# Optimization experiments

Measured on AMD Instinct MI355X. Metric: run time of the kernel, lower is better.

## Reference

```python
import jax, jax.numpy as jnp
import numpy as np

# Pangu-Weather EarthSpecificBlock, layer-1 config
WZ, WH, WW = 2, 6, 12          # window size (z, lat, lon)
Z, H, W = 8, 91, 180           # token grid after patch embedding
C = 192                        # token dim
HEADS = 6
B = 1
PAD_TOP, PAD_BOT = 2, 3        # lat 91 -> 96 (CustomPad3d, centered)
ZP, HP, WP = 8, 96, 180        # padded grid
NWB = (ZP // WZ) * (HP // WH)  # 64 bias windows (z*lat)
N = WZ * WH * WW               # 144 tokens per window


def earth_position_index():
    zi = np.arange(WZ); zj = -np.arange(WZ) * WZ
    hi = np.arange(WH); hj = -np.arange(WH) * WH
    w = np.arange(WW)
    c1 = np.stack(np.meshgrid(zi, hi, w, indexing='ij')).reshape(3, -1)
    c2 = np.stack(np.meshgrid(zj, hj, w, indexing='ij')).reshape(3, -1)
    coords = (c1[:, :, None] - c2[:, None, :]).transpose(1, 2, 0).astype(np.int64)
    coords[:, :, 2] += WW - 1
    coords[:, :, 1] *= 2 * WW - 1
    coords[:, :, 0] *= (2 * WW - 1) * WH * WH
    return coords.sum(-1)  # (N, N) int indices into bias table

POS_IDX = jnp.asarray(earth_position_index())


def layer_norm(x, w, b, eps=1e-5):
    mu = x.mean(-1, keepdims=True)
    var = ((x - mu) ** 2).mean(-1, keepdims=True)
    return (x - mu) * jax.lax.rsqrt(var + eps) * w + b


def setup_inputs() -> dict:
    key = jax.random.key(0)
    ks = jax.random.split(key, 8)
    f = lambda k, s: jax.random.normal(k, s, jnp.float32) * 0.02
    return {
        "x": jax.random.normal(ks[0], (B, Z * H * W, C), jnp.float32),
        "qkv_w": f(ks[1], (3 * C, C)),
        "qkv_b": jnp.zeros((3 * C,), jnp.float32),
        "proj_w": f(ks[2], (C, C)),
        "proj_b": jnp.zeros((C,), jnp.float32),
        "bias_table": f(ks[3], ((2 * WW - 1) * WH * WH * WZ * WZ, NWB, HEADS)),
        "norm1_w": jnp.ones((C,), jnp.float32),
        "norm1_b": jnp.zeros((C,), jnp.float32),
        "norm2_w": jnp.ones((C,), jnp.float32),
        "norm2_b": jnp.zeros((C,), jnp.float32),
        "mlp_w1": f(ks[4], (4 * C, C)),
        "mlp_b1": jnp.zeros((4 * C,), jnp.float32),
        "mlp_w2": f(ks[5], (C, 4 * C)),
        "mlp_b2": jnp.zeros((C,), jnp.float32),
        "roll": 0,
    }


def reference(x, qkv_w, qkv_b, proj_w, proj_b, bias_table,
              norm1_w, norm1_b, norm2_w, norm2_b,
              mlp_w1, mlp_b1, mlp_w2, mlp_b2, roll):
    shortcut = x  # (B, L, C)
    hd = C // HEADS
    scale = hd ** -0.5
    xs = x.reshape(B, Z, H, W, C)
    xs = jnp.pad(xs, ((0, 0), (0, 0), (PAD_TOP, PAD_BOT), (0, 0), (0, 0)))
    # window partition: (B, ZP, HP, WP, C) -> (nb, N, C), windows ordered (z, lat, lon)
    xw = xs.reshape(B, ZP // WZ, WZ, HP // WH, WH, WP // WW, WW, C)
    xw = xw.transpose(0, 1, 3, 5, 2, 4, 6, 7).reshape(-1, N, C)
    nb = xw.shape[0]  # B * 64 * 15 = 960
    qkv = (xw @ qkv_w.T + qkv_b).reshape(nb, N, 3, HEADS, hd).transpose(2, 0, 3, 1, 4)
    q, k, v = qkv[0] * scale, qkv[1], qkv[2]  # each (nb, HEADS, N, hd)
    att = jnp.einsum('bhnd,bhmd->bhnm', q, k)  # (nb, HEADS, N, N)
    # earth-specific bias gathered via position index
    bias = bias_table[POS_IDX]                 # (N, N, NWB, HEADS)
    bias = bias.transpose(2, 3, 0, 1)          # (NWB, HEADS, N, N)
    # nb = B * NWB * n_lon_windows, NWB is the leading window factor
    att = att.reshape(B, NWB, -1, HEADS, N, N) + bias[None, :, None]
    att = jax.nn.softmax(att, axis=-1).reshape(nb, HEADS, N, N)
    out = jnp.einsum('bhnm,bhmd->bnhd', att, v).reshape(nb, N, C)
    out = out @ proj_w.T + proj_b
    # window reverse + crop padding
    out = out.reshape(B, ZP // WZ, HP // WH, WP // WW, WZ, WH, WW, C)
    out = out.transpose(0, 1, 4, 2, 5, 3, 6, 7).reshape(B, ZP, HP, WP, C)
    out = out[:, :, PAD_TOP:HP - PAD_BOT, :, :].reshape(B, -1, C)
    # post-norm residual (Pangu): x = shortcut + norm1(attn); x = x + norm2(mlp(x))
    x1 = shortcut + layer_norm(out, norm1_w, norm1_b)
    h1 = jax.nn.gelu(x1 @ mlp_w1.T + mlp_b1, approximate=False)
    mlp_out = h1 @ mlp_w2.T + mlp_b2
    return x1 + layer_norm(mlp_out, norm2_w, norm2_b)
```

## Files before the change

kernel.cpp:

```cpp
#include <hip/hip_runtime.h>
#include <hip/hip_bf16.h>

typedef __hip_bfloat16 bf16;
#define DEVI __device__ __forceinline__

typedef __bf16 bf16x8 __attribute__((ext_vector_type(8)));
typedef __bf16 bf16x4 __attribute__((ext_vector_type(4)));
typedef float  f32x4  __attribute__((ext_vector_type(4)));

DEVI float bf2f(bf16 v) { return __bfloat162float(v); }
DEVI bf16 f2bf(float v) { return __float2bfloat16(v); }

DEVI unsigned short bfbits(float x) {
    bf16 h = __float2bfloat16(x);
    return *reinterpret_cast<unsigned short*>(&h);
}
DEVI unsigned int pack2(float x, float y) {
    return (unsigned int)bfbits(x) | ((unsigned int)bfbits(y) << 16);
}
DEVI bf16x8 pack8(float4 lo, float4 hi) {
    union { unsigned int u[4]; bf16x8 v; } z;
    z.u[0] = pack2(lo.x, lo.y); z.u[1] = pack2(lo.z, lo.w);
    z.u[2] = pack2(hi.x, hi.y); z.u[3] = pack2(hi.z, hi.w);
    return z.v;
}
DEVI bf16x8 ld8h(const bf16* p) {
    bf16x4 lo = *(const bf16x4*)p;
    bf16x4 hi = *(const bf16x4*)(p + 4);
    return __builtin_shufflevector(lo, hi, 0, 1, 2, 3, 4, 5, 6, 7);
}

__global__ __launch_bounds__(256) void prep_attn_w(
    const float* __restrict__ qkv_w, const float* __restrict__ qkv_b,
    bf16* __restrict__ qkv_wb, float* __restrict__ qkv_bb)
{
    const float scale = 0.17677669529663687f;
    int idx = blockIdx.x * 256 + threadIdx.x;
    if (idx < 110592) {
        int c = idx % 192, d = idx / 192;
        int h = d / 96, q2 = d - h * 96, seg = q2 >> 5, rr = q2 & 31;
        float v = qkv_w[(size_t)(seg * 192 + h * 32 + rr) * 192 + c];
        if (seg == 0) v *= scale;
        qkv_wb[idx] = f2bf(v);
    }
    if (idx < 576) {
        int h = idx / 96, q2 = idx - h * 96, seg = q2 >> 5, rr = q2 & 31;
        float b = qkv_b[seg * 192 + h * 32 + rr];
        if (seg == 0) b *= scale;
        qkv_bb[idx] = b;
    }
}

__global__ __launch_bounds__(256) void prep_bias(
    const float* __restrict__ bias_table, bf16* __restrict__ biasT)
{
    int idx = blockIdx.x * 256 + threadIdx.x;
    if (idx >= 7962624) return;
    int t = idx % 144;
    int k = (idx / 144) % 144;
    int r2 = idx / 20736;
    int h = r2 % 6, wb = r2 / 6;
    int tzq = t / 72, thq = (t / 12) % 6, twq = t % 12;
    int tzk = k / 72, thk = (k / 12) % 6, twk = k % 12;
    int bidx = (tzq + 2 * tzk) * 828 + (thq + 6 * thk) * 23 + (twq - twk + 11);
    biasT[idx] = f2bf(bias_table[(size_t)(bidx * 64 + wb) * 6 + h]);
}

__global__ __launch_bounds__(256, 4) void attn_mfma_kernel(
    const float* __restrict__ x, const bf16* __restrict__ qkv_wb,
    const float* __restrict__ qkv_bb, const bf16* __restrict__ biasT,
    bf16* __restrict__ attn_out)
{
    __shared__ alignas(16) char sm[30976];
    bf16* Qs  = (bf16*)sm;
    bf16* Ks  = (bf16*)(sm + 10368);
    bf16* VTs = (bf16*)(sm + 20736);

    const int tid  = threadIdx.x;
    const int wave = tid >> 6;
    const int lane = tid & 63;
    const int quad = lane >> 4;
    const int l15  = lane & 15;

    const int bid     = blockIdx.x;
    const int logical = (bid & 7) * 720 + (bid >> 3);
    const int wi      = logical / 6;
    const int head    = logical % 6;
    const int ww_  = wi % 15;
    const int hw   = (wi / 15) % 16;
    const int zw   = wi / 240;
    const int wb   = zw * 16 + hw;

    for (int i = tid; i < 512; i += 256) {
        int d = i >> 4, c = i & 15;
        VTs[d * 160 + 144 + c] = f2bf(0.f);
    }

    for (int i = 0; i < 3; ++i) {
        int mt = wave + 4 * i;
        if (mt < 9) {
            int t  = mt * 16 + l15;
            int tz = t / 72, rr = t - tz * 72;
            int th = rr / 12, tw = rr - th * 12;
            int lat = hw * 6 + th - 2;
            bool valid = (lat >= 0 && lat < 91);
            size_t base = ((size_t)((zw * 2 + tz) * 91 + (valid ? lat : 0)) * 180
                           + ww_ * 12 + tw) * 192;
            bf16x8 af[6];
#pragma unroll
            for (int ks = 0; ks < 6; ++ks) {
                float4 lo = make_float4(0.f, 0.f, 0.f, 0.f);
                float4 hi = make_float4(0.f, 0.f, 0.f, 0.f);
                if (valid) {
                    lo = *(const float4*)(x + base + ks * 32 + quad * 8);
                    hi = *(const float4*)(x + base + ks * 32 + quad * 8 + 4);
                }
                af[ks] = pack8(lo, hi);
            }
            for (int nt = 0; nt < 6; ++nt) {
                const bf16* wrow = qkv_wb + (size_t)(head * 96 + nt * 16 + l15) * 192;
                bf16x8 bw[6];
#pragma unroll
                for (int ks = 0; ks < 6; ++ks)
                    bw[ks] = *(const bf16x8*)(wrow + ks * 32 + quad * 8);
                float bias = qkv_bb[head * 96 + nt * 16 + l15];

                f32x4 acc = (f32x4){0.f, 0.f, 0.f, 0.f};
#pragma unroll
                for (int ks = 0; ks < 6; ++ks)
                    acc = __builtin_amdgcn_mfma_f32_16x16x32_bf16(
                        af[ks], bw[ks], acc, 0, 0, 0);
#pragma unroll
                for (int r = 0; r < 4; ++r) {
                    float v = acc[r] + bias;
                    int tok = mt * 16 + quad * 4 + r;
                    if (nt < 2)      Qs[tok * 36 + nt * 16 + l15] = f2bf(v);
                    else if (nt < 4) Ks[tok * 36 + (nt - 2) * 16 + l15] = f2bf(v);
                    else             VTs[((nt - 4) * 16 + l15) * 160 + tok] = f2bf(v);
                }
            }
        }
    }
    __syncthreads();

    const bf16* bt = biasT + (size_t)(wb * 6 + head) * 20736;

    for (int i = 0; i < 3; ++i) {
        int nti = wave + 4 * i;
        if (nti >= 9) continue;

        bf16x8 qb = ld8h(Qs + (nti * 16 + l15) * 36 + quad * 8);

        f32x4 st[9];
#pragma unroll
        for (int mt = 0; mt < 9; ++mt) {
            bf16x8 ka = ld8h(Ks + (mt * 16 + l15) * 36 + quad * 8);
            st[mt] = (f32x4){0.f, 0.f, 0.f, 0.f};
            st[mt] = __builtin_amdgcn_mfma_f32_16x16x32_bf16(
                ka, qb, st[mt], 0, 0, 0);
        }

#pragma unroll
        for (int mt = 0; mt < 9; ++mt)
#pragma unroll
            for (int r = 0; r < 4; ++r)
                st[mt][r] += bf2f(bt[(mt * 16 + quad * 4 + r) * 144
                                     + nti * 16 + l15]);

        float mx = -1e30f;
#pragma unroll
        for (int mt = 0; mt < 9; ++mt)
#pragma unroll
            for (int r = 0; r < 4; ++r) mx = fmaxf(mx, st[mt][r]);
        mx = fmaxf(mx, __shfl_xor(mx, 16, 64));
        mx = fmaxf(mx, __shfl_xor(mx, 32, 64));
        float s = 0.f;
#pragma unroll
        for (int mt = 0; mt < 9; ++mt)
#pragma unroll
            for (int r = 0; r < 4; ++r) {
                float e = __expf(st[mt][r] - mx);
                st[mt][r] = e;
                s += e;
            }
        s += __shfl_xor(s, 16, 64);
        s += __shfl_xor(s, 32, 64);
        float inv = 1.f / s;
#pragma unroll
        for (int mt = 0; mt < 9; ++mt)
#pragma unroll
            for (int r = 0; r < 4; ++r) st[mt][r] *= inv;

        f32x4 oa[2];
        oa[0] = (f32x4){0.f, 0.f, 0.f, 0.f};
        oa[1] = (f32x4){0.f, 0.f, 0.f, 0.f};
#pragma unroll
        for (int ks = 0; ks < 5; ++ks) {
            unsigned A0 = pack2(st[2 * ks][0], st[2 * ks][1]);
            unsigned A1 = pack2(st[2 * ks][2], st[2 * ks][3]);
            unsigned B0 = 0u, B1 = 0u;
            if (ks < 4) {
                B0 = pack2(st[2 * ks + 1][0], st[2 * ks + 1][1]);
                B1 = pack2(st[2 * ks + 1][2], st[2 * ks + 1][3]);
            }
            bool lo2 = quad < 2;
            unsigned Z0 = lo2 ? A0 : B0, Z1 = lo2 ? A1 : B1;
            unsigned Y0 = lo2 ? B0 : A0, Y1 = lo2 ? B1 : A1;
            unsigned s16_0 = __shfl_xor((int)Z0, 16, 64);
            unsigned s16_1 = __shfl_xor((int)Z1, 16, 64);
            unsigned s32_0 = __shfl_xor((int)Y0, 32, 64);
            unsigned s32_1 = __shfl_xor((int)Y1, 32, 64);
            unsigned s48_0 = __shfl_xor((int)Y0, 48, 64);
            unsigned s48_1 = __shfl_xor((int)Y1, 48, 64);
            union { unsigned u[4]; bf16x8 v; } fr;
            fr.u[0] = (quad == 0) ? Z0 : (quad == 1) ? s48_0 : (quad == 2) ? s32_0 : s16_0;
            fr.u[1] = (quad == 0) ? Z1 : (quad == 1) ? s48_1 : (quad == 2) ? s32_1 : s16_1;
            fr.u[2] = (quad == 0) ? s16_0 : (quad == 1) ? s32_0 : (quad == 2) ? s48_0 : Z0;
            fr.u[3] = (quad == 0) ? s16_1 : (quad == 1) ? s32_1 : (quad == 2) ? s48_1 : Z1;
#pragma unroll
            for (int n2 = 0; n2 < 2; ++n2) {
                bf16x8 vb = *(const bf16x8*)(VTs + (n2 * 16 + l15) * 160
                                             + ks * 32 + quad * 8);
                oa[n2] = __builtin_amdgcn_mfma_f32_16x16x32_bf16(
                    fr.v, vb, oa[n2], 0, 0, 0);
            }
        }

#pragma unroll
        for (int n2 = 0; n2 < 2; ++n2)
#pragma unroll
            for (int r = 0; r < 4; ++r) {
                int tok = nti * 16 + quad * 4 + r;
                attn_out[(size_t)(wi * 144 + tok) * 192 + (head << 5) + n2 * 16 + l15]
                    = f2bf(oa[n2][r]);
            }
    }
}

__global__ __launch_bounds__(256, 2) void proj_mfma_kernel(
    const bf16* __restrict__ attn, const float* __restrict__ proj_w,
    const float* __restrict__ proj_b, const float* __restrict__ xin,
    const float* __restrict__ n1w, const float* __restrict__ n1b,
    bf16* __restrict__ x1out)
{
    __shared__ alignas(16) char sm[56320];
    bf16*  Xs     = (bf16*)sm;
    float* wsum   = (float*)(sm + 51200);
    float* wsq    = (float*)(sm + 53248);
    float* mean_s = (float*)(sm + 55296);
    float* rstd_s = (float*)(sm + 55808);

    const int tid  = threadIdx.x;
    const int wave = tid >> 6;
    const int lane = tid & 63;
    const int quad = lane >> 4;
    const int l15  = lane & 15;
    const long tok0 = (long)blockIdx.x * 128;
    const int colw = wave * 48;

    for (int i = tid; i < 128 * 24; i += 256) {
        int r = i / 24, c4 = i - r * 24;
        long l = tok0 + r;
        uint4 v = make_uint4(0u, 0u, 0u, 0u);
        if (l < 131040) {
            int li  = (int)l;
            int z   = li / 16380, rem = li - z * 16380;
            int lat = rem / 180, lon = rem - lat * 180;
            int latp = lat + 2;
            int zw = z >> 1, tz = z & 1;
            int hw = latp / 6, th = latp - hw * 6;
            int wwn = lon / 12, tw = lon - wwn * 12;
            int wi = (zw * 16 + hw) * 15 + wwn;
            int t  = (tz * 6 + th) * 12 + tw;
            v = *(const uint4*)(attn + (size_t)(wi * 144 + t) * 192 + c4 * 8);
        }
        *(uint4*)(Xs + r * 200 + c4 * 8) = v;
    }
    __syncthreads();

    f32x4 o[3][8];
#pragma unroll
    for (int nt = 0; nt < 3; ++nt)
#pragma unroll
        for (int mt = 0; mt < 8; ++mt)
            o[nt][mt] = (f32x4){0.f, 0.f, 0.f, 0.f};

#pragma unroll
    for (int ks = 0; ks < 6; ++ks) {
        bf16x8 wfr[3];
#pragma unroll
        for (int nt = 0; nt < 3; ++nt) {
            const float* wp = proj_w + (size_t)(colw + nt * 16 + l15) * 192
                            + ks * 32 + quad * 8;
            float4 lo = *(const float4*)wp;
            float4 hi = *(const float4*)(wp + 4);
            wfr[nt] = pack8(lo, hi);
        }
#pragma unroll
        for (int mt = 0; mt < 8; ++mt) {
            bf16x8 a = *(const bf16x8*)(Xs + (mt * 16 + l15) * 200 + ks * 32 + quad * 8);
#pragma unroll
            for (int nt = 0; nt < 3; ++nt)
                o[nt][mt] = __builtin_amdgcn_mfma_f32_16x16x32_bf16(
                    a, wfr[nt], o[nt][mt], 0, 0, 0);
        }
    }

    float pbv[3], gw[3], gb[3];
#pragma unroll
    for (int nt = 0; nt < 3; ++nt) {
        int c = colw + nt * 16 + l15;
        pbv[nt] = proj_b[c];
        gw[nt]  = n1w[c];
        gb[nt]  = n1b[c];
    }
#pragma unroll
    for (int nt = 0; nt < 3; ++nt)
#pragma unroll
        for (int mt = 0; mt < 8; ++mt)
#pragma unroll
            for (int r = 0; r < 4; ++r)
                o[nt][mt][r] += pbv[nt];

#pragma unroll
    for (int mt = 0; mt < 8; ++mt) {
#pragma unroll
        for (int r = 0; r < 4; ++r) {
            float p = o[0][mt][r] + o[1][mt][r] + o[2][mt][r];
            float q = o[0][mt][r] * o[0][mt][r] + o[1][mt][r] * o[1][mt][r]
                    + o[2][mt][r] * o[2][mt][r];
#pragma unroll
            for (int m_ = 1; m_ < 16; m_ <<= 1) {
                p += __shfl_xor(p, m_, 64);
                q += __shfl_xor(q, m_, 64);
            }
            if (l15 == 0) {
                int row = mt * 16 + quad * 4 + r;
                wsum[row * 4 + wave] = p;
                wsq [row * 4 + wave] = q;
            }
        }
    }
    __syncthreads();
    if (tid < 128) {
        float s  = wsum[tid * 4] + wsum[tid * 4 + 1] + wsum[tid * 4 + 2] + wsum[tid * 4 + 3];
        float ss = wsq [tid * 4] + wsq [tid * 4 + 1] + wsq [tid * 4 + 2] + wsq [tid * 4 + 3];
        float m = s * (1.f / 192.f);
        float var = ss * (1.f / 192.f) - m * m;
        mean_s[tid] = m;
        rstd_s[tid] = rsqrtf(fmaxf(var, 0.f) + 1e-5f);
    }
    __syncthreads();

#pragma unroll
    for (int mt = 0; mt < 8; ++mt) {
#pragma unroll
        for (int r = 0; r < 4; ++r) {
            int row = mt * 16 + quad * 4 + r;
            long tok = tok0 + row;
            if (tok < 131040) {
                float m = mean_s[row], rsd = rstd_s[row];
#pragma unroll
                for (int nt = 0; nt < 3; ++nt) {
                    int c = colw + nt * 16 + l15;
                    float val = (o[nt][mt][r] - m) * rsd * gw[nt] + gb[nt]
                              + xin[(size_t)tok * 192 + c];
                    x1out[(size_t)tok * 192 + c] = f2bf(val);
                }
            }
        }
    }
}

__global__ __launch_bounds__(256) void prep_weights(
    const float* __restrict__ w1, const float* __restrict__ w2,
    unsigned int* __restrict__ w1b, unsigned int* __restrict__ w2b)
{
    int i = blockIdx.x * 256 + threadIdx.x;
    if (i < 73728) {
        w1b[i] = pack2(w1[2 * i], w1[2 * i + 1]);
    } else {
        int j = i - 73728;
        w2b[j] = pack2(w2[2 * j], w2[2 * j + 1]);
    }
}

__global__ __launch_bounds__(256, 2) void mlp_mfma_kernel(
    const bf16* __restrict__ x1, const bf16* __restrict__ w1b,
    const float* __restrict__ b1, const bf16* __restrict__ w2b,
    const float* __restrict__ b2, const float* __restrict__ n2w,
    const float* __restrict__ n2b, float* __restrict__ out)
{
    __shared__ alignas(16) char sm[53760];
    bf16*  Xs     = (bf16*)sm;
    bf16*  Hs     = (bf16*)(sm + 25600);
    float* wsum   = (float*)(sm + 51200);
    float* wsq    = (float*)(sm + 52224);
    float* mean_s = (float*)(sm + 53248);
    float* rstd_s = (float*)(sm + 53504);

    const int tid  = threadIdx.x;
    const int wave = tid >> 6;
    const int lane = tid & 63;
    const int quad = lane >> 4;
    const int l15  = lane & 15;
    const long tok0 = (long)blockIdx.x * 64;
    const int colw = wave * 48;

    for (int i = tid; i < 64 * 24; i += 256) {
        int r = i / 24, c8 = i - r * 24;
        uint4 v = make_uint4(0u, 0u, 0u, 0u);
        if (tok0 + r < 131040)
            v = *(const uint4*)(x1 + (tok0 + r) * 192 + (size_t)c8 * 8);
        *(uint4*)(Xs + r * 200 + c8 * 8) = v;
    }
    __syncthreads();

    bf16x8 af[4][6];
#pragma unroll
    for (int mt = 0; mt < 4; ++mt)
#pragma unroll
        for (int ks = 0; ks < 6; ++ks)
            af[mt][ks] = *(const bf16x8*)(Xs + (mt * 16 + l15) * 200 + ks * 32 + quad * 8);

    f32x4 o[3][4];
#pragma unroll
    for (int nt = 0; nt < 3; ++nt)
#pragma unroll
        for (int mt = 0; mt < 4; ++mt)
            o[nt][mt] = (f32x4){0.f, 0.f, 0.f, 0.f};

    for (int nc = 0; nc < 4; ++nc) {
        f32x4 g[3][4];
#pragma unroll
        for (int nt = 0; nt < 3; ++nt)
#pragma unroll
            for (int mt = 0; mt < 4; ++mt)
                g[nt][mt] = (f32x4){0.f, 0.f, 0.f, 0.f};
        const int h0 = nc * 192 + colw;
#pragma unroll
        for (int ks = 0; ks < 6; ++ks) {
            bf16x8 bfr[3];
#pragma unroll
            for (int nt = 0; nt < 3; ++nt)
                bfr[nt] = *(const bf16x8*)(w1b + (size_t)(h0 + nt * 16 + l15) * 192 + ks * 32 + quad * 8);
#pragma unroll
            for (int nt = 0; nt < 3; ++nt)
#pragma unroll
                for (int mt = 0; mt < 4; ++mt)
                    g[nt][mt] = __builtin_amdgcn_mfma_f32_16x16x32_bf16(
                        af[mt][ks], bfr[nt], g[nt][mt], 0, 0, 0);
        }
        __syncthreads();

#pragma unroll
        for (int nt = 0; nt < 3; ++nt) {
            float bb = b1[h0 + nt * 16 + l15];
            int hcol = colw + nt * 16 + l15;
#pragma unroll
            for (int mt = 0; mt < 4; ++mt) {
#pragma unroll
                for (int r = 0; r < 4; ++r) {
                    float v = g[nt][mt][r] + bb;
                    float u = v * (0.7978845608028654f + 0.035677408136300125f * v * v);
                    float e = __expf(2.f * u);
                    float t = 1.f - 2.f / (e + 1.f);
                    float gl = 0.5f * v * (1.f + t);
                    Hs[(mt * 16 + quad * 4 + r) * 200 + hcol] = f2bf(gl);
                }
            }
        }
        __syncthreads();

#pragma unroll
        for (int ks = 0; ks < 6; ++ks) {
            bf16x8 hf[4];
#pragma unroll
            for (int mt = 0; mt < 4; ++mt)
                hf[mt] = *(const bf16x8*)(Hs + (mt * 16 + l15) * 200 + ks * 32 + quad * 8);
            bf16x8 wf[3];
#pragma unroll
            for (int nt = 0; nt < 3; ++nt)
                wf[nt] = *(const bf16x8*)(w2b + (size_t)(colw + nt * 16 + l15) * 768 + nc * 192 + ks * 32 + quad * 8);
#pragma unroll
            for (int nt = 0; nt < 3; ++nt)
#pragma unroll
                for (int mt = 0; mt < 4; ++mt)
                    o[nt][mt] = __builtin_amdgcn_mfma_f32_16x16x32_bf16(
                        hf[mt], wf[nt], o[nt][mt], 0, 0, 0);
        }
    }

    float b2v[3], gw[3], gb[3];
#pragma unroll
    for (int nt = 0; nt < 3; ++nt) {
        int c = colw + nt * 16 + l15;
        b2v[nt] = b2[c];
        gw[nt] = n2w[c];
        gb[nt] = n2b[c];
    }
#pragma unroll
    for (int nt = 0; nt < 3; ++nt)
#pragma unroll
        for (int mt = 0; mt < 4; ++mt)
#pragma unroll
            for (int r = 0; r < 4; ++r)
                o[nt][mt][r] += b2v[nt];

#pragma unroll
    for (int mt = 0; mt < 4; ++mt) {
#pragma unroll
        for (int r = 0; r < 4; ++r) {
            float p = o[0][mt][r] + o[1][mt][r] + o[2][mt][r];
            float q = o[0][mt][r] * o[0][mt][r] + o[1][mt][r] * o[1][mt][r]
                    + o[2][mt][r] * o[2][mt][r];
#pragma unroll
            for (int m_ = 1; m_ < 16; m_ <<= 1) {
                p += __shfl_xor(p, m_, 64);
                q += __shfl_xor(q, m_, 64);
            }
            if (l15 == 0) {
                int row = mt * 16 + quad * 4 + r;
                wsum[row * 4 + wave] = p;
                wsq [row * 4 + wave] = q;
            }
        }
    }
    __syncthreads();
    if (tid < 64) {
        float s  = wsum[tid * 4] + wsum[tid * 4 + 1] + wsum[tid * 4 + 2] + wsum[tid * 4 + 3];
        float ss = wsq [tid * 4] + wsq [tid * 4 + 1] + wsq [tid * 4 + 2] + wsq [tid * 4 + 3];
        float m = s * (1.f / 192.f);
        float var = ss * (1.f / 192.f) - m * m;
        mean_s[tid] = m;
        rstd_s[tid] = rsqrtf(fmaxf(var, 0.f) + 1e-5f);
    }
    __syncthreads();

#pragma unroll
    for (int mt = 0; mt < 4; ++mt) {
#pragma unroll
        for (int r = 0; r < 4; ++r) {
            int row = mt * 16 + quad * 4 + r;
            long tok = tok0 + row;
            if (tok < 131040) {
                float m = mean_s[row], rsd = rstd_s[row];
#pragma unroll
                for (int nt = 0; nt < 3; ++nt) {
                    int c = colw + nt * 16 + l15;
                    float val = (o[nt][mt][r] - m) * rsd * gw[nt] + gb[nt]
                              + bf2f(Xs[row * 200 + c]);
                    out[tok * 192 + c] = val;
                }
            }
        }
    }
}

extern "C" void kernel_launch(void* const* d_in, const int* in_sizes, int n_in,
                              void* d_out, int out_size, void* d_ws, size_t ws_size,
                              hipStream_t stream) {
    (void)in_sizes; (void)n_in; (void)out_size; (void)ws_size;
    const float* x          = (const float*)d_in[0];
    const float* qkv_w      = (const float*)d_in[1];
    const float* qkv_b      = (const float*)d_in[2];
    const float* proj_w     = (const float*)d_in[3];
    const float* proj_b     = (const float*)d_in[4];
    const float* bias_table = (const float*)d_in[5];
    const float* n1w        = (const float*)d_in[6];
    const float* n1b        = (const float*)d_in[7];
    const float* n2w        = (const float*)d_in[8];
    const float* n2b        = (const float*)d_in[9];
    const float* w1         = (const float*)d_in[10];
    const float* b1         = (const float*)d_in[11];
    const float* w2         = (const float*)d_in[12];
    const float* b2         = (const float*)d_in[13];
    float* out = (float*)d_out;

    bf16*  attn_ws = (bf16*)d_ws;
    bf16*  x1_ws   = (bf16*)((char*)d_ws + 53084160);
    bf16*  w1b     = (bf16*)d_ws;
    bf16*  w2b     = (bf16*)((char*)d_ws + 294912);
    bf16*  qkv_wb  = (bf16*)((char*)d_ws + 53084160);
    float* qkv_bb  = (float*)((char*)d_ws + 53305344);
    bf16*  biasT   = (bf16*)((char*)d_ws + 53307648);

    prep_attn_w<<<432, 256, 0, stream>>>(qkv_w, qkv_b, qkv_wb, qkv_bb);
    prep_bias<<<31104, 256, 0, stream>>>(bias_table, biasT);
    attn_mfma_kernel<<<5760, 256, 0, stream>>>(x, qkv_wb, qkv_bb, biasT, attn_ws);
    proj_mfma_kernel<<<1024, 256, 0, stream>>>(attn_ws, proj_w, proj_b, x, n1w, n1b, x1_ws);
    prep_weights<<<576, 256, 0, stream>>>(w1, w2, (unsigned int*)w1b, (unsigned int*)w2b);
    mlp_mfma_kernel<<<2048, 256, 0, stream>>>(x1_ws, w1b, b1, w2b, b2, n2w, n2b, out);
}
```

Before: 756.2 us.

## Split QKV projection out of attention into a separate GEMM kernel

```diff
diff --git a/kernel.cpp b/kernel.cpp
--- a/kernel.cpp
+++ b/kernel.cpp
@@ -10,6 +10,7 @@
 
 DEVI float bf2f(bf16 v) { return __bfloat162float(v); }
 DEVI bf16 f2bf(float v) { return __float2bfloat16(v); }
+DEVI float bfu2f(unsigned short u) { return __uint_as_float((unsigned)u << 16); }
 
 DEVI unsigned short bfbits(float x) {
     bf16 h = __float2bfloat16(x);
@@ -56,17 +57,232 @@
 {
     int idx = blockIdx.x * 256 + threadIdx.x;
     if (idx >= 7962624) return;
-    int t = idx % 144;
-    int k = (idx / 144) % 144;
+    int m = idx % 144;
+    int n = (idx / 144) % 144;
     int r2 = idx / 20736;
     int h = r2 % 6, wb = r2 / 6;
-    int tzq = t / 72, thq = (t / 12) % 6, twq = t % 12;
-    int tzk = k / 72, thk = (k / 12) % 6, twk = k % 12;
-    int bidx = (tzq + 2 * tzk) * 828 + (thq + 6 * thk) * 23 + (twq - twk + 11);
+    int tzn = n / 72, thn = (n / 12) % 6, twn = n % 12;
+    int tzm = m / 72, thm = (m / 12) % 6, twm = m % 12;
+    int bidx = (tzn + 2 * tzm) * 828 + (thn + 6 * thm) * 23 + (twn - twm + 11);
     biasT[idx] = f2bf(bias_table[(size_t)(bidx * 64 + wb) * 6 + h]);
 }
 
-__global__ __launch_bounds__(256, 4) void attn_mfma_kernel(
+__global__ __launch_bounds__(256) void zero_vtpad(bf16* __restrict__ vt)
+{
+    int idx = blockIdx.x * 256 + threadIdx.x;
+    if (idx >= 368640) return;
+    int row = idx >> 1, half = idx & 1;
+    uint4 z = make_uint4(0u, 0u, 0u, 0u);
+    *(uint4*)(vt + (size_t)row * 160 + 144 + half * 8) = z;
+}
+
+__global__ __launch_bounds__(256, 2) void qkv_gemm_kernel(
+    const float* __restrict__ x, const bf16* __restrict__ qkv_wb,
+    const float* __restrict__ qkv_bb, bf16* __restrict__ qk,
+    bf16* __restrict__ vt)
+{
+    __shared__ alignas(16) bf16 Xs[48 * 200];
+    const int tid  = threadIdx.x;
+    const int wave = tid >> 6;
+    const int lane = tid & 63;
+    const int quad = lane >> 4;
+    const int l15  = lane & 15;
+    const int b    = blockIdx.x;
+    const int wi   = b / 3, tblk = b % 3;
+    const int ww_  = wi % 15;
+    const int hw   = (wi / 15) % 16;
+    const int zw   = wi / 240;
+
+    for (int i = tid; i < 48 * 24; i += 256) {
+        int r = i / 24, c8 = i - r * 24;
+        int t  = tblk * 48 + r;
+        int tz = t / 72, rr = t - tz * 72;
+        int th = rr / 12, tw = rr - th * 12;
+        int lat = hw * 6 + th - 2;
+        bool valid = (lat >= 0 && lat < 91);
+        uint4 val = make_uint4(0u, 0u, 0u, 0u);
+        if (valid) {
+            size_t base = ((size_t)((zw * 2 + tz) * 91 + lat) * 180
+                           + ww_ * 12 + tw) * 192;
+            float4 lo = *(const float4*)(x + base + c8 * 8);
+            float4 hi = *(const float4*)(x + base + c8 * 8 + 4);
+            bf16x8 p = pack8(lo, hi);
+            val = *(uint4*)&p;
+        }
+        *(uint4*)(Xs + r * 200 + c8 * 8) = val;
+    }
+    __syncthreads();
+
+    bf16x8 af[3][6];
+#pragma unroll
+    for (int mt = 0; mt < 3; ++mt)
+#pragma unroll
+        for (int ks = 0; ks < 6; ++ks)
+            af[mt][ks] = *(const bf16x8*)(Xs + (mt * 16 + l15) * 200 + ks * 32 + quad * 8);
+
+    const int colw = wave * 144;
+    for (int nt = 0; nt < 9; ++nt) {
+        int c0  = colw + nt * 16;
+        int h   = c0 / 96, q20 = c0 % 96;
+        int seg = q20 >> 5, rr0 = q20 & 31;
+        const bf16* wrow = qkv_wb + (size_t)(h * 96 + q20 + l15) * 192;
+        bf16x8 wfr[6];
+#pragma unroll
+        for (int ks = 0; ks < 6; ++ks)
+            wfr[ks] = *(const bf16x8*)(wrow + ks * 32 + quad * 8);
+        float bias = qkv_bb[h * 96 + q20 + l15];
+
+        f32x4 acc[3];
+#pragma unroll
+        for (int mt = 0; mt < 3; ++mt) acc[mt] = (f32x4){0.f, 0.f, 0.f, 0.f};
+#pragma unroll
+        for (int ks = 0; ks < 6; ++ks)
+#pragma unroll
+            for (int mt = 0; mt < 3; ++mt)
+                acc[mt] = __builtin_amdgcn_mfma_f32_16x16x32_bf16(
+                    af[mt][ks], wfr[ks], acc[mt], 0, 0, 0);
+
+        if (seg < 2) {
+            bf16* dst = qk + (size_t)((wi * 6 + h) * 2 + seg) * 4608 + rr0 + l15;
+#pragma unroll
+            for (int mt = 0; mt < 3; ++mt)
+#pragma unroll
+                for (int r = 0; r < 4; ++r) {
+                    int tok = tblk * 48 + mt * 16 + quad * 4 + r;
+                    dst[tok * 32] = f2bf(acc[mt][r] + bias);
+                }
+        } else {
+            bf16* dst = vt + ((size_t)(wi * 6 + h) * 32 + rr0 + l15) * 160;
+#pragma unroll
+            for (int mt = 0; mt < 3; ++mt)
+#pragma unroll
+                for (int r = 0; r < 4; ++r) {
+                    int tok = tblk * 48 + mt * 16 + quad * 4 + r;
+                    dst[tok] = f2bf(acc[mt][r] + bias);
+                }
+        }
+    }
+}
+
+__global__ __launch_bounds__(256, 4) void attn_slim_kernel(
+    const bf16* __restrict__ qk, const bf16* __restrict__ vt,
+    const bf16* __restrict__ biasT, bf16* __restrict__ attn_out)
+{
+    const int tid  = threadIdx.x;
+    const int wave = tid >> 6;
+    const int lane = tid & 63;
+    const int quad = lane >> 4;
+    const int l15  = lane & 15;
+
+    const int bid     = blockIdx.x;
+    const int logical = (bid & 7) * 720 + (bid >> 3);
+    const int wi      = logical / 6;
+    const int head    = logical % 6;
+    const int hw = (wi / 15) % 16;
+    const int zw = wi / 240;
+    const int wb = zw * 16 + hw;
+
+    const bf16* Qg = qk + (size_t)((wi * 6 + head) * 2) * 4608;
+    const bf16* Kg = Qg + 4608;
+    const bf16* Vg = vt + (size_t)(wi * 6 + head) * 32 * 160;
+    const bf16* bt = biasT + (size_t)(wb * 6 + head) * 20736;
+
+    for (int i = 0; i < 3; ++i) {
+        int nti = wave + 4 * i;
+        if (nti >= 9) continue;
+
+        bf16x8 qb = *(const bf16x8*)(Qg + (nti * 16 + l15) * 32 + quad * 8);
+
+        f32x4 st[9];
+#pragma unroll
+        for (int mt = 0; mt < 9; ++mt) {
+            bf16x8 ka = *(const bf16x8*)(Kg + (mt * 16 + l15) * 32 + quad * 8);
+            st[mt] = (f32x4){0.f, 0.f, 0.f, 0.f};
+            st[mt] = __builtin_amdgcn_mfma_f32_16x16x32_bf16(
+                ka, qb, st[mt], 0, 0, 0);
+        }
+
+        const bf16* brow = bt + (size_t)(nti * 16 + l15) * 144 + quad * 4;
+#pragma unroll
+        for (int mt = 0; mt < 9; ++mt) {
+            union { bf16x4 v; unsigned short u[4]; } bb_;
+            bb_.v = *(const bf16x4*)(brow + mt * 16);
+#pragma unroll
+            for (int r = 0; r < 4; ++r)
+                st[mt][r] += bfu2f(bb_.u[r]);
+        }
+
+        float mx = -1e30f;
+#pragma unroll
+        for (int mt = 0; mt < 9; ++mt)
+#pragma unroll
+            for (int r = 0; r < 4; ++r) mx = fmaxf(mx, st[mt][r]);
+        mx = fmaxf(mx, __shfl_xor(mx, 16, 64));
+        mx = fmaxf(mx, __shfl_xor(mx, 32, 64));
+        float s = 0.f;
+#pragma unroll
+        for (int mt = 0; mt < 9; ++mt)
+#pragma unroll
+            for (int r = 0; r < 4; ++r) {
+                float e = __expf(st[mt][r] - mx);
+                st[mt][r] = e;
+                s += e;
+            }
+        s += __shfl_xor(s, 16, 64);
+        s += __shfl_xor(s, 32, 64);
+        float inv = 1.f / s;
+#pragma unroll
+        for (int mt = 0; mt < 9; ++mt)
+#pragma unroll
+            for (int r = 0; r < 4; ++r) st[mt][r] *= inv;
+
+        f32x4 oa[2];
+        oa[0] = (f32x4){0.f, 0.f, 0.f, 0.f};
+        oa[1] = (f32x4){0.f, 0.f, 0.f, 0.f};
+#pragma unroll
+        for (int ks = 0; ks < 5; ++ks) {
+            unsigned A0 = pack2(st[2 * ks][0], st[2 * ks][1]);
+            unsigned A1 = pack2(st[2 * ks][2], st[2 * ks][3]);
+            unsigned B0 = 0u, B1 = 0u;
+            if (ks < 4) {
+                B0 = pack2(st[2 * ks + 1][0], st[2 * ks + 1][1]);
+                B1 = pack2(st[2 * ks + 1][2], st[2 * ks + 1][3]);
+            }
+            bool lo2 = quad < 2;
+            unsigned Z0 = lo2 ? A0 : B0, Z1 = lo2 ? A1 : B1;
+            unsigned Y0 = lo2 ? B0 : A0, Y1 = lo2 ? B1 : A1;
+            unsigned s16_0 = __shfl_xor((int)Z0, 16, 64);
+            unsigned s16_1 = __shfl_xor((int)Z1, 16, 64);
+            unsigned s32_0 = __shfl_xor((int)Y0, 32, 64);
+            unsigned s32_1 = __shfl_xor((int)Y1, 32, 64);
+            unsigned s48_0 = __shfl_xor((int)Y0, 48, 64);
+            unsigned s48_1 = __shfl_xor((int)Y1, 48, 64);
+            union { unsigned u[4]; bf16x8 v; } fr;
+            fr.u[0] = (quad == 0) ? Z0 : (quad == 1) ? s48_0 : (quad == 2) ? s32_0 : s16_0;
+            fr.u[1] = (quad == 0) ? Z1 : (quad == 1) ? s48_1 : (quad == 2) ? s32_1 : s16_1;
+            fr.u[2] = (quad == 0) ? s16_0 : (quad == 1) ? s32_0 : (quad == 2) ? s48_0 : Z0;
+            fr.u[3] = (quad == 0) ? s16_1 : (quad == 1) ? s32_1 : (quad == 2) ? s48_1 : Z1;
+#pragma unroll
+            for (int n2 = 0; n2 < 2; ++n2) {
+                bf16x8 vb = *(const bf16x8*)(Vg + (n2 * 16 + l15) * 160
+                                             + ks * 32 + quad * 8);
+                oa[n2] = __builtin_amdgcn_mfma_f32_16x16x32_bf16(
+                    fr.v, vb, oa[n2], 0, 0, 0);
+            }
+        }
+
+#pragma unroll
+        for (int n2 = 0; n2 < 2; ++n2)
+#pragma unroll
+            for (int r = 0; r < 4; ++r) {
+                int tok = nti * 16 + quad * 4 + r;
+                attn_out[(size_t)(wi * 144 + tok) * 192 + (head << 5) + n2 * 16 + l15]
+                    = f2bf(oa[n2][r]);
+            }
+    }
+}
+
+__global__ __launch_bounds__(256, 4) void attn_fused_kernel(
     const float* __restrict__ x, const bf16* __restrict__ qkv_wb,
     const float* __restrict__ qkv_bb, const bf16* __restrict__ biasT,
     bf16* __restrict__ attn_out)
@@ -160,12 +376,15 @@
                 ka, qb, st[mt], 0, 0, 0);
         }
 
-#pragma unroll
-        for (int mt = 0; mt < 9; ++mt)
+        const bf16* brow = bt + (size_t)(nti * 16 + l15) * 144 + quad * 4;
+#pragma unroll
+        for (int mt = 0; mt < 9; ++mt) {
+            union { bf16x4 v; unsigned short u[4]; } bb_;
+            bb_.v = *(const bf16x4*)(brow + mt * 16);
 #pragma unroll
             for (int r = 0; r < 4; ++r)
-                st[mt][r] += bf2f(bt[(mt * 16 + quad * 4 + r) * 144
-                                     + nti * 16 + l15]);
+                st[mt][r] += bfu2f(bb_.u[r]);
+        }
 
         float mx = -1e30f;
 #pragma unroll
@@ -560,7 +779,7 @@
 extern "C" void kernel_launch(void* const* d_in, const int* in_sizes, int n_in,
                               void* d_out, int out_size, void* d_ws, size_t ws_size,
                               hipStream_t stream) {
-    (void)in_sizes; (void)n_in; (void)out_size; (void)ws_size;
+    (void)in_sizes; (void)n_in; (void)out_size;
     const float* x          = (const float*)d_in[0];
     const float* qkv_w      = (const float*)d_in[1];
     const float* qkv_b      = (const float*)d_in[2];
@@ -577,18 +796,40 @@
     const float* b2         = (const float*)d_in[13];
     float* out = (float*)d_out;
 
-    bf16*  attn_ws = (bf16*)d_ws;
-    bf16*  x1_ws   = (bf16*)((char*)d_ws + 53084160);
-    bf16*  w1b     = (bf16*)d_ws;
-    bf16*  w2b     = (bf16*)((char*)d_ws + 294912);
-    bf16*  qkv_wb  = (bf16*)((char*)d_ws + 53084160);
-    float* qkv_bb  = (float*)((char*)d_ws + 53305344);
-    bf16*  biasT   = (bf16*)((char*)d_ws + 53307648);
-
-    prep_attn_w<<<432, 256, 0, stream>>>(qkv_w, qkv_b, qkv_wb, qkv_bb);
-    prep_bias<<<31104, 256, 0, stream>>>(bias_table, biasT);
-    attn_mfma_kernel<<<5760, 256, 0, stream>>>(x, qkv_wb, qkv_bb, biasT, attn_ws);
-    proj_mfma_kernel<<<1024, 256, 0, stream>>>(attn_ws, proj_w, proj_b, x, n1w, n1b, x1_ws);
-    prep_weights<<<576, 256, 0, stream>>>(w1, w2, (unsigned int*)w1b, (unsigned int*)w2b);
-    mlp_mfma_kernel<<<2048, 256, 0, stream>>>(x1_ws, w1b, b1, w2b, b2, n2w, n2b, out);
-}
+    const size_t SPLIT_WS = 234383616ULL;
+    if (ws_size >= SPLIT_WS) {
+        bf16*  attn_ws = (bf16*)d_ws;
+        bf16*  qkg     = (bf16*)((char*)d_ws + 53084160);
+        bf16*  vtg     = (bf16*)((char*)d_ws + 159252480);
+        bf16*  biasT   = (bf16*)((char*)d_ws + 218234880);
+        bf16*  qkv_wb  = (bf16*)((char*)d_ws + 234160128);
+        float* qkv_bb  = (float*)((char*)d_ws + 234381312);
+        bf16*  x1_ws   = (bf16*)((char*)d_ws + 53084160);
+        bf16*  w1b     = (bf16*)((char*)d_ws + 103403520);
+        bf16*  w2b     = (bf16*)((char*)d_ws + 103698432);
+
+        prep_attn_w<<<432, 256, 0, stream>>>(qkv_w, qkv_b, qkv_wb, qkv_bb);
+        prep_bias<<<31104, 256, 0, stream>>>(bias_table, biasT);
+        zero_vtpad<<<1440, 256, 0, stream>>>(vtg);
+        qkv_gemm_kernel<<<2880, 256, 0, stream>>>(x, qkv_wb, qkv_bb, qkg, vtg);
+        attn_slim_kernel<<<5760, 256, 0, stream>>>(qkg, vtg, biasT, attn_ws);
+        proj_mfma_kernel<<<1024, 256, 0, stream>>>(attn_ws, proj_w, proj_b, x, n1w, n1b, x1_ws);
+        prep_weights<<<576, 256, 0, stream>>>(w1, w2, (unsigned int*)w1b, (unsigned int*)w2b);
+        mlp_mfma_kernel<<<2048, 256, 0, stream>>>(x1_ws, w1b, b1, w2b, b2, n2w, n2b, out);
+    } else {
+        bf16*  attn_ws = (bf16*)d_ws;
+        bf16*  x1_ws   = (bf16*)((char*)d_ws + 53084160);
+        bf16*  w1b     = (bf16*)d_ws;
+        bf16*  w2b     = (bf16*)((char*)d_ws + 294912);
+        bf16*  qkv_wb  = (bf16*)((char*)d_ws + 53084160);
+        float* qkv_bb  = (float*)((char*)d_ws + 53305344);
+        bf16*  biasT   = (bf16*)((char*)d_ws + 53307648);
+
+        prep_attn_w<<<432, 256, 0, stream>>>(qkv_w, qkv_b, qkv_wb, qkv_bb);
+        prep_bias<<<31104, 256, 0, stream>>>(bias_table, biasT);
+        attn_fused_kernel<<<5760, 256, 0, stream>>>(x, qkv_wb, qkv_bb, biasT, attn_ws);
+        proj_mfma_kernel<<<1024, 256, 0, stream>>>(attn_ws, proj_w, proj_b, x, n1w, n1b, x1_ws);
+        prep_weights<<<576, 256, 0, stream>>>(w1, w2, (unsigned int*)w1b, (unsigned int*)w2b);
+        mlp_mfma_kernel<<<2048, 256, 0, stream>>>(x1_ws, w1b, b1, w2b, b2, n2w, n2b, out);
+    }
+}
```

New measurement: 716.4 us. 1.06x faster.
